# Kernel optimization log

Measured on AMD Instinct MI355X. Metric: run time of the kernel, lower is better.

Reference implementation:

```python
import jax, jax.numpy as jnp
import numpy as np

N, K, D_IN, D_OUT = 50000, 16, 256, 256
LN_EPS = 1e-5


def setup_inputs() -> dict:
    key = jax.random.key(0)
    k1, k2, k3, k4 = jax.random.split(key, 4)
    features = jax.random.normal(k1, (N, D_IN), dtype=jnp.float32)
    neighbors = jax.random.randint(k2, (N, K), 0, N, dtype=jnp.int64)
    importance_weights = jax.random.uniform(k3, (N, K), dtype=jnp.float32)
    # Linear(in_channels, out_channels): weight stored as [D_IN, D_OUT] for x @ W + b
    W = jax.random.normal(k4, (D_IN, D_OUT), dtype=jnp.float32) * (1.0 / np.sqrt(D_IN))
    b = jnp.zeros((D_OUT,), dtype=jnp.float32)
    gamma = jnp.ones((D_OUT,), dtype=jnp.float32)
    beta = jnp.zeros((D_OUT,), dtype=jnp.float32)
    return {"features": features, "neighbors": neighbors,
            "importance_weights": importance_weights,
            "W": W, "b": b, "gamma": gamma, "beta": beta}


def reference(features, neighbors, importance_weights, W, b, gamma, beta):
    # Gather neighbor features: [N, K, D_IN]
    neigh_feats = features[neighbors]
    # Linear transform: [N, K, D_OUT]
    transformed = jnp.einsum('nkd,df->nkf', neigh_feats, W) + b
    # Normalize importance weights per node; zero-sum fallback = uniform mean
    wsum = jnp.sum(importance_weights, axis=-1, keepdims=True)  # [N, 1]
    norm_w = jnp.where(wsum == 0.0,
                       jnp.full_like(importance_weights, 1.0 / K),
                       importance_weights / jnp.where(wsum == 0.0, 1.0, wsum))
    # Importance-weighted sum over neighbors: [N, D_OUT]
    agg = jnp.einsum('nkf,nk->nf', transformed, norm_w)
    # LayerNorm over feature dim (torch: biased variance, eps=1e-5)
    mean = jnp.mean(agg, axis=-1, keepdims=True)
    var = jnp.mean((agg - mean) ** 2, axis=-1, keepdims=True)
    out = (agg - mean) * jax.lax.rsqrt(var + LN_EPS) * gamma + beta
    return out
```

## Files before the change

kernel.cpp:

```cpp
#include <hip/hip_runtime.h>


#define NN   50000
#define KNB  16
#define D    256

typedef __attribute__((ext_vector_type(8))) short short8;
typedef __attribute__((ext_vector_type(4))) float f32x4;

static __device__ __forceinline__ unsigned short f2bf(float x) {
    unsigned int u = __float_as_uint(x);
    return (unsigned short)((u + 0x7FFFu + ((u >> 16) & 1u)) >> 16);
}
static __device__ __forceinline__ float bf2f(unsigned short h) {
    return __uint_as_float((unsigned int)h << 16);
}

__global__ __launch_bounds__(256) void convert_w(const float* __restrict__ Wm,
                                                 unsigned short* __restrict__ wtp) {
    const int g    = blockIdx.x * 256 + threadIdx.x;
    const int lane = g & 63;
    const int kb32 = (g >> 6) & 7;
    const int c    = g >> 9;
    const int n    = c * 16 + (lane & 15);
    const int k0   = kb32 * 32 + (lane >> 4) * 8;
    short8 v;
    #pragma unroll
    for (int j = 0; j < 8; ++j) v[j] = (short)f2bf(Wm[(size_t)(k0 + j) * D + n]);
    *(short8*)(wtp + (size_t)g * 8) = v;
}

__global__ __launch_bounds__(256) void convert_feat(const float* __restrict__ feat,
                                                    unsigned short* __restrict__ featb) {
    const size_t g = (size_t)blockIdx.x * 256 + threadIdx.x;
    const float4 a = *(const float4*)(feat + g * 8);
    const float4 b = *(const float4*)(feat + g * 8 + 4);
    short8 o;
    o[0] = (short)f2bf(a.x); o[1] = (short)f2bf(a.y);
    o[2] = (short)f2bf(a.z); o[3] = (short)f2bf(a.w);
    o[4] = (short)f2bf(b.x); o[5] = (short)f2bf(b.y);
    o[6] = (short)f2bf(b.z); o[7] = (short)f2bf(b.w);
    *(short8*)(featb + g * 8) = o;
}

__global__ __launch_bounds__(256, 8) void pool_b(const unsigned short* __restrict__ featb,
                                                 const int*   __restrict__ nbr,
                                                 const float* __restrict__ iw,
                                                 unsigned short* __restrict__ aggb) {
    const int  t    = threadIdx.x;
    const int  lane = t & 63;
    const int  wq   = t >> 6;
    const long n    = (long)blockIdx.x * 4 + wq;

    float ws = 0.f;
    #pragma unroll
    for (int k = 0; k < KNB; ++k) ws += iw[n * KNB + k];
    const bool  zs  = (ws == 0.f);
    const float inv = zs ? (1.f / KNB) : (1.f / ws);

    float4 p = make_float4(0.f, 0.f, 0.f, 0.f);
    #pragma unroll 1
    for (int kb = 0; kb < KNB; kb += 8) {
        int   idx[8];
        float w[8];
        #pragma unroll
        for (int k = 0; k < 8; ++k) {
            idx[k] = nbr[n * KNB + kb + k];
            w[k]   = iw [n * KNB + kb + k];
        }
        #pragma unroll
        for (int k = 0; k < 8; ++k) {
            const float   wk = zs ? inv : (w[k] * inv);
            const ushort4 u  = *(const ushort4*)(featb + (size_t)idx[k] * D + lane * 4);
            p.x += wk * bf2f(u.x); p.y += wk * bf2f(u.y);
            p.z += wk * bf2f(u.z); p.w += wk * bf2f(u.w);
        }
    }
    ushort4 o;
    o.x = f2bf(p.x); o.y = f2bf(p.y); o.z = f2bf(p.z); o.w = f2bf(p.w);
    *(ushort4*)(aggb + (size_t)n * 512 + lane * 4) = o;
}

__global__ __launch_bounds__(256, 8) void pool_f(const float* __restrict__ feat,
                                                 const int*   __restrict__ nbr,
                                                 const float* __restrict__ iw,
                                                 unsigned short* __restrict__ aggb) {
    const int  t    = threadIdx.x;
    const int  lane = t & 63;
    const int  wq   = t >> 6;
    const long n    = (long)blockIdx.x * 4 + wq;
    float ws = 0.f;
    #pragma unroll
    for (int k = 0; k < KNB; ++k) ws += iw[n * KNB + k];
    const bool  zs  = (ws == 0.f);
    const float inv = zs ? (1.f / KNB) : (1.f / ws);
    float4 p = make_float4(0.f, 0.f, 0.f, 0.f);
    #pragma unroll 1
    for (int kb = 0; kb < KNB; kb += 8) {
        int idx[8]; float w[8];
        #pragma unroll
        for (int k = 0; k < 8; ++k) { idx[k] = nbr[n*KNB+kb+k]; w[k] = iw[n*KNB+kb+k]; }
        #pragma unroll
        for (int k = 0; k < 8; ++k) {
            const float  wk = zs ? inv : (w[k] * inv);
            const float4 f  = *(const float4*)(feat + (size_t)idx[k] * D + lane * 4);
            p.x += wk*f.x; p.y += wk*f.y; p.z += wk*f.z; p.w += wk*f.w;
        }
    }
    ushort4 o;
    o.x = f2bf(p.x); o.y = f2bf(p.y); o.z = f2bf(p.z); o.w = f2bf(p.w);
    *(ushort4*)(aggb + (size_t)n * 512 + lane * 4) = o;
}

__global__ __launch_bounds__(256, 4) void gemm_ln(const unsigned short* __restrict__ aggb,
                                                  const unsigned short* __restrict__ wtp,
                                                  const float* __restrict__ bias,
                                                  const float* __restrict__ gamma,
                                                  const float* __restrict__ beta,
                                                  float* __restrict__ out) {
    const int t       = threadIdx.x;
    const int lane    = t & 63;
    const int wq      = t >> 6;
    const int quad    = lane >> 4;
    const int l15     = lane & 15;
    const int rowbase = blockIdx.x * 64 + wq * 16;

    const int arow = min(rowbase + l15, NN - 1);
    const unsigned short* aptr = aggb + (size_t)arow * 512 + quad * 8;
    const short8* wv = (const short8*)wtp;

    f32x4 acc[16];
    #pragma unroll
    for (int c = 0; c < 16; ++c) acc[c] = (f32x4){0.f, 0.f, 0.f, 0.f};

    #pragma unroll
    for (int kb = 0; kb < 8; ++kb) {
        const short8 a = *(const short8*)(aptr + kb * 32);
        #pragma unroll
        for (int c = 0; c < 16; ++c) {
            const short8 b = wv[(size_t)(c * 8 + kb) * 64 + lane];
            acc[c] = __builtin_amdgcn_mfma_f32_16x16x32_bf16(a, b, acc[c], 0, 0, 0);
        }
    }

    float bv[16];
    #pragma unroll
    for (int c = 0; c < 16; ++c) bv[c] = bias[c * 16 + l15];

    #pragma unroll
    for (int j = 0; j < 4; ++j) {
        float s = 0.f, sq = 0.f;
        #pragma unroll
        for (int c = 0; c < 16; ++c) {
            const float v = acc[c][j] + bv[c];
            s += v; sq += v * v;
        }
        #pragma unroll
        for (int off = 1; off < 16; off <<= 1) {
            s  += __shfl_xor(s,  off, 64);
            sq += __shfl_xor(sq, off, 64);
        }
        const float mean = s * (1.f / D);
        const float var  = sq * (1.f / D) - mean * mean;
        const float rstd = rsqrtf(var + 1e-5f);
        const int   r    = rowbase + quad * 4 + j;
        if (r < NN) {
            float* op = out + (size_t)r * D + l15;
            #pragma unroll
            for (int c = 0; c < 16; ++c) {
                const float v = acc[c][j] + bv[c];
                op[c * 16] = (v - mean) * rstd * gamma[c * 16 + l15] + beta[c * 16 + l15];
            }
        }
    }
}

extern "C" void kernel_launch(void* const* d_in, const int* in_sizes, int n_in,
                              void* d_out, int out_size, void* d_ws, size_t ws_size,
                              hipStream_t stream) {
    const float* feat = (const float*)d_in[0];
    const int*   nbr  = (const int*)d_in[1];
    const float* iw   = (const float*)d_in[2];
    const float* Wm   = (const float*)d_in[3];
    const float* b    = (const float*)d_in[4];
    const float* g    = (const float*)d_in[5];
    const float* be   = (const float*)d_in[6];
    float*       out  = (float*)d_out;

    unsigned short* wtp   = (unsigned short*)d_ws;
    unsigned short* featb = (unsigned short*)((char*)d_ws + 131072);
    unsigned short* aggb  = (unsigned short*)d_out;

    const size_t need = 131072 + (size_t)NN * D * 2;

    convert_w<<<dim3(32), dim3(256), 0, stream>>>(Wm, wtp);
    if (ws_size >= need) {
        convert_feat<<<dim3(6250),   dim3(256), 0, stream>>>(feat, featb);
        pool_b      <<<dim3(NN / 4), dim3(256), 0, stream>>>(featb, nbr, iw, aggb);
    } else {
        pool_f      <<<dim3(NN / 4), dim3(256), 0, stream>>>(feat, nbr, iw, aggb);
    }
    gemm_ln<<<dim3((NN + 63) / 64), dim3(256), 0, stream>>>(aggb, wtp, b, g, be, out);
}
```

Baseline: 204.7 us.

## Fuse pooling with GEMM+LayerNorm via LDS and merge conversion kernels

Merges the weight and feature bf16 conversions into one launch, then fuses the neighbor pooling with the MFMA GEMM and LayerNorm. Each single-wave block pools 16 rows into shared memory and runs the GEMM on them directly, which removes the global round trip for the aggregated rows and two launches. Output rows are staged through LDS so they can be written as coalesced float4 stores. In exchange, 64-thread blocks with a low occupancy hint may leave less latency hiding for the random gathers. The fp32 fallback path used when the workspace is too small is removed.

```diff
diff --git a/kernel.cpp b/kernel.cpp
--- a/kernel.cpp
+++ b/kernel.cpp
@@ -4,6 +4,8 @@
 #define NN   50000
 #define KNB  16
 #define D    256
+#define RPB  16
+#define ASTR 264
 
 typedef __attribute__((ext_vector_type(8))) short short8;
 typedef __attribute__((ext_vector_type(4))) float f32x4;
@@ -16,117 +18,80 @@
     return __uint_as_float((unsigned int)h << 16);
 }
 
-__global__ __launch_bounds__(256) void convert_w(const float* __restrict__ Wm,
-                                                 unsigned short* __restrict__ wtp) {
-    const int g    = blockIdx.x * 256 + threadIdx.x;
-    const int lane = g & 63;
-    const int kb32 = (g >> 6) & 7;
-    const int c    = g >> 9;
-    const int n    = c * 16 + (lane & 15);
-    const int k0   = kb32 * 32 + (lane >> 4) * 8;
-    short8 v;
-    #pragma unroll
-    for (int j = 0; j < 8; ++j) v[j] = (short)f2bf(Wm[(size_t)(k0 + j) * D + n]);
-    *(short8*)(wtp + (size_t)g * 8) = v;
+__global__ __launch_bounds__(256) void convert_all(const float* __restrict__ feat,
+                                                   const float* __restrict__ Wm,
+                                                   unsigned short* __restrict__ featb,
+                                                   unsigned short* __restrict__ wtp) {
+    if (blockIdx.x < 6250) {
+        const size_t g = (size_t)blockIdx.x * 256 + threadIdx.x;
+        const float4 a = *(const float4*)(feat + g * 8);
+        const float4 b = *(const float4*)(feat + g * 8 + 4);
+        short8 o;
+        o[0] = (short)f2bf(a.x); o[1] = (short)f2bf(a.y);
+        o[2] = (short)f2bf(a.z); o[3] = (short)f2bf(a.w);
+        o[4] = (short)f2bf(b.x); o[5] = (short)f2bf(b.y);
+        o[6] = (short)f2bf(b.z); o[7] = (short)f2bf(b.w);
+        *(short8*)(featb + g * 8) = o;
+    } else {
+        const int g    = (blockIdx.x - 6250) * 256 + threadIdx.x;
+        const int lane = g & 63;
+        const int kb   = (g >> 6) & 7;
+        const int c    = g >> 9;
+        const int n    = c * 16 + (lane & 15);
+        const int k0   = kb * 32 + (lane >> 4) * 8;
+        short8 v;
+        #pragma unroll
+        for (int j = 0; j < 8; ++j) v[j] = (short)f2bf(Wm[(size_t)(k0 + j) * D + n]);
+        *(short8*)(wtp + (size_t)g * 8) = v;
+    }
 }
 
-__global__ __launch_bounds__(256) void convert_feat(const float* __restrict__ feat,
-                                                    unsigned short* __restrict__ featb) {
-    const size_t g = (size_t)blockIdx.x * 256 + threadIdx.x;
-    const float4 a = *(const float4*)(feat + g * 8);
-    const float4 b = *(const float4*)(feat + g * 8 + 4);
-    short8 o;
-    o[0] = (short)f2bf(a.x); o[1] = (short)f2bf(a.y);
-    o[2] = (short)f2bf(a.z); o[3] = (short)f2bf(a.w);
-    o[4] = (short)f2bf(b.x); o[5] = (short)f2bf(b.y);
-    o[6] = (short)f2bf(b.z); o[7] = (short)f2bf(b.w);
-    *(short8*)(featb + g * 8) = o;
-}
+__global__ __launch_bounds__(64, 3) void fused(const unsigned short* __restrict__ featb,
+                                               const int*   __restrict__ nbr,
+                                               const float* __restrict__ iw,
+                                               const unsigned short* __restrict__ wtp,
+                                               const float* __restrict__ bias,
+                                               const float* __restrict__ gamma,
+                                               const float* __restrict__ beta,
+                                               float* __restrict__ out) {
+    __shared__ unsigned short sAgg[RPB * ASTR];
 
-__global__ __launch_bounds__(256, 8) void pool_b(const unsigned short* __restrict__ featb,
-                                                 const int*   __restrict__ nbr,
-                                                 const float* __restrict__ iw,
-                                                 unsigned short* __restrict__ aggb) {
-    const int  t    = threadIdx.x;
-    const int  lane = t & 63;
-    const int  wq   = t >> 6;
-    const long n    = (long)blockIdx.x * 4 + wq;
+    const int  lane    = threadIdx.x;
+    const int  quad    = lane >> 4;
+    const int  l15     = lane & 15;
+    const long rowbase = (long)blockIdx.x * RPB;
 
-    float ws = 0.f;
-    #pragma unroll
-    for (int k = 0; k < KNB; ++k) ws += iw[n * KNB + k];
-    const bool  zs  = (ws == 0.f);
-    const float inv = zs ? (1.f / KNB) : (1.f / ws);
+    #pragma unroll 1
+    for (int i = 0; i < RPB; ++i) {
+        const long n = rowbase + i;
+        int   idx[KNB];
+        float w[KNB];
+        #pragma unroll
+        for (int k = 0; k < KNB; ++k) {
+            idx[k] = nbr[n * KNB + k];
+            w[k]   = iw [n * KNB + k];
+        }
+        float ws = 0.f;
+        #pragma unroll
+        for (int k = 0; k < KNB; ++k) ws += w[k];
+        const bool  zs  = (ws == 0.f);
+        const float inv = zs ? (1.f / KNB) : (1.f / ws);
 
-    float4 p = make_float4(0.f, 0.f, 0.f, 0.f);
-    #pragma unroll 1
-    for (int kb = 0; kb < KNB; kb += 8) {
-        int   idx[8];
-        float w[8];
+        float4 p = make_float4(0.f, 0.f, 0.f, 0.f);
         #pragma unroll
-        for (int k = 0; k < 8; ++k) {
-            idx[k] = nbr[n * KNB + kb + k];
-            w[k]   = iw [n * KNB + kb + k];
-        }
-        #pragma unroll
-        for (int k = 0; k < 8; ++k) {
+        for (int k = 0; k < KNB; ++k) {
             const float   wk = zs ? inv : (w[k] * inv);
             const ushort4 u  = *(const ushort4*)(featb + (size_t)idx[k] * D + lane * 4);
             p.x += wk * bf2f(u.x); p.y += wk * bf2f(u.y);
             p.z += wk * bf2f(u.z); p.w += wk * bf2f(u.w);
         }
+        ushort4 o;
+        o.x = f2bf(p.x); o.y = f2bf(p.y); o.z = f2bf(p.z); o.w = f2bf(p.w);
+        *(ushort4*)(sAgg + i * ASTR + lane * 4) = o;
     }
-    ushort4 o;
-    o.x = f2bf(p.x); o.y = f2bf(p.y); o.z = f2bf(p.z); o.w = f2bf(p.w);
-    *(ushort4*)(aggb + (size_t)n * 512 + lane * 4) = o;
-}
+    __syncthreads();
 
-__global__ __launch_bounds__(256, 8) void pool_f(const float* __restrict__ feat,
-                                                 const int*   __restrict__ nbr,
-                                                 const float* __restrict__ iw,
-                                                 unsigned short* __restrict__ aggb) {
-    const int  t    = threadIdx.x;
-    const int  lane = t & 63;
-    const int  wq   = t >> 6;
-    const long n    = (long)blockIdx.x * 4 + wq;
-    float ws = 0.f;
-    #pragma unroll
-    for (int k = 0; k < KNB; ++k) ws += iw[n * KNB + k];
-    const bool  zs  = (ws == 0.f);
-    const float inv = zs ? (1.f / KNB) : (1.f / ws);
-    float4 p = make_float4(0.f, 0.f, 0.f, 0.f);
-    #pragma unroll 1
-    for (int kb = 0; kb < KNB; kb += 8) {
-        int idx[8]; float w[8];
-        #pragma unroll
-        for (int k = 0; k < 8; ++k) { idx[k] = nbr[n*KNB+kb+k]; w[k] = iw[n*KNB+kb+k]; }
-        #pragma unroll
-        for (int k = 0; k < 8; ++k) {
-            const float  wk = zs ? inv : (w[k] * inv);
-            const float4 f  = *(const float4*)(feat + (size_t)idx[k] * D + lane * 4);
-            p.x += wk*f.x; p.y += wk*f.y; p.z += wk*f.z; p.w += wk*f.w;
-        }
-    }
-    ushort4 o;
-    o.x = f2bf(p.x); o.y = f2bf(p.y); o.z = f2bf(p.z); o.w = f2bf(p.w);
-    *(ushort4*)(aggb + (size_t)n * 512 + lane * 4) = o;
-}
-
-__global__ __launch_bounds__(256, 4) void gemm_ln(const unsigned short* __restrict__ aggb,
-                                                  const unsigned short* __restrict__ wtp,
-                                                  const float* __restrict__ bias,
-                                                  const float* __restrict__ gamma,
-                                                  const float* __restrict__ beta,
-                                                  float* __restrict__ out) {
-    const int t       = threadIdx.x;
-    const int lane    = t & 63;
-    const int wq      = t >> 6;
-    const int quad    = lane >> 4;
-    const int l15     = lane & 15;
-    const int rowbase = blockIdx.x * 64 + wq * 16;
-
-    const int arow = min(rowbase + l15, NN - 1);
-    const unsigned short* aptr = aggb + (size_t)arow * 512 + quad * 8;
+    const unsigned short* ap = sAgg + (size_t)l15 * ASTR + quad * 8;
     const short8* wv = (const short8*)wtp;
 
     f32x4 acc[16];
@@ -135,7 +100,7 @@
 
     #pragma unroll
     for (int kb = 0; kb < 8; ++kb) {
-        const short8 a = *(const short8*)(aptr + kb * 32);
+        const short8 a = *(const short8*)(ap + kb * 32);
         #pragma unroll
         for (int c = 0; c < 16; ++c) {
             const short8 b = wv[(size_t)(c * 8 + kb) * 64 + lane];
@@ -143,10 +108,14 @@
         }
     }
 
-    float bv[16];
+    float bv[16], gv[16], btv[16];
     #pragma unroll
-    for (int c = 0; c < 16; ++c) bv[c] = bias[c * 16 + l15];
-
+    for (int c = 0; c < 16; ++c) {
+        bv[c]  = bias [c * 16 + l15];
+        gv[c]  = gamma[c * 16 + l15];
+        btv[c] = beta [c * 16 + l15];
+    }
+    float* fsh = (float*)sAgg;
     #pragma unroll
     for (int j = 0; j < 4; ++j) {
         float s = 0.f, sq = 0.f;
@@ -163,15 +132,18 @@
         const float mean = s * (1.f / D);
         const float var  = sq * (1.f / D) - mean * mean;
         const float rstd = rsqrtf(var + 1e-5f);
-        const int   r    = rowbase + quad * 4 + j;
-        if (r < NN) {
-            float* op = out + (size_t)r * D + l15;
-            #pragma unroll
-            for (int c = 0; c < 16; ++c) {
-                const float v = acc[c][j] + bv[c];
-                op[c * 16] = (v - mean) * rstd * gamma[c * 16 + l15] + beta[c * 16 + l15];
-            }
+        #pragma unroll
+        for (int c = 0; c < 16; ++c)
+            fsh[quad * 265 + c * 16 + l15] =
+                (acc[c][j] + bv[c] - mean) * rstd * gv[c] + btv[c];
+        __syncthreads();
+        #pragma unroll
+        for (int p = 0; p < 4; ++p) {
+            const long r = rowbase + p * 4 + j;
+            const float4 vv = *(const float4*)(fsh + p * 265 + lane * 4);
+            *(float4*)(out + r * D + lane * 4) = vv;
         }
+        __syncthreads();
     }
 }
 
@@ -189,16 +161,8 @@
 
     unsigned short* wtp   = (unsigned short*)d_ws;
     unsigned short* featb = (unsigned short*)((char*)d_ws + 131072);
-    unsigned short* aggb  = (unsigned short*)d_out;
 
-    const size_t need = 131072 + (size_t)NN * D * 2;
-
-    convert_w<<<dim3(32), dim3(256), 0, stream>>>(Wm, wtp);
-    if (ws_size >= need) {
-        convert_feat<<<dim3(6250),   dim3(256), 0, stream>>>(feat, featb);
-        pool_b      <<<dim3(NN / 4), dim3(256), 0, stream>>>(featb, nbr, iw, aggb);
-    } else {
-        pool_f      <<<dim3(NN / 4), dim3(256), 0, stream>>>(feat, nbr, iw, aggb);
-    }
-    gemm_ln<<<dim3((NN + 63) / 64), dim3(256), 0, stream>>>(aggb, wtp, b, g, be, out);
+    convert_all<<<dim3(6250 + 32), dim3(256), 0, stream>>>(feat, Wm, featb, wtp);
+    fused      <<<dim3(NN / RPB),  dim3(64),  0, stream>>>(featb, nbr, iw, wtp,
+                                                           b, g, be, out);
 }
```

New measurement: 284.2 us. 38.9% more time.
